# Kernel tuning notes

Measured on AMD Instinct MI355X. Metric: run time of the kernel, lower is better.

The kernel has to match this reference:

```python
import jax, jax.numpy as jnp
import numpy as np

N = 50000
E = 800000
D_IN = 96
D_OUT = 128


def setup_inputs() -> dict:
    key = jax.random.key(0)
    k1, k2, k3, k4, k5 = jax.random.split(key, 5)
    x = jax.random.normal(k1, (N, D_IN), dtype=jnp.float32)
    edge_index = jax.random.randint(k2, (2, E), 0, N, dtype=jnp.int32)
    s = 1.0 / np.sqrt(D_IN)
    # lin_l: applied to aggregated neighbor features (has bias in PyG SAGEConv)
    W_l = jax.random.uniform(k3, (D_OUT, D_IN), jnp.float32, -s, s)
    b_l = jax.random.uniform(k4, (D_OUT,), jnp.float32, -s, s)
    # lin_r: root/self weight (no bias)
    W_r = jax.random.uniform(k5, (D_OUT, D_IN), jnp.float32, -s, s)
    return {"x": x, "edge_index": edge_index, "W_l": W_l, "b_l": b_l, "W_r": W_r}


def reference(x, edge_index, W_l, b_l, W_r):
    src, dst = edge_index[0], edge_index[1]
    # gather source features, mean-aggregate onto targets
    msg = x[src]  # [E, D_IN]
    summed = jax.ops.segment_sum(msg, dst, num_segments=N)  # [N, D_IN]
    count = jax.ops.segment_sum(jnp.ones((E,), x.dtype), dst, num_segments=N)
    agg = summed / jnp.maximum(count, 1.0)[:, None]
    # SAGEConv: lin_l(agg) + lin_r(x), then layer-level ReLU
    out = agg @ W_l.T + b_l + x @ W_r.T
    return jax.nn.relu(out)
```

## Files before the change

kernel.cpp:

```cpp
#include <hip/hip_runtime.h>
#include <hip/hip_bf16.h>

#define N_NODES 50000
#define N_EDGES 800000
#define D_IN 96
#define D_OUT 128
#define CAP 64

#define NPB 64
#define N_BINS ((N_NODES + NPB - 1) / NPB)
#define CAP_SUB 24
#define PART_EPB 3125
#define PART_BLOCKS (N_EDGES / PART_EPB)
#define PART_SLOTS 13

#define CONV_THREADS (N_NODES * 12)
#define CONV_BLOCKS ((CONV_THREADS + 255) / 256)
#define WCONV_BLOCKS 12

#define AG_BLOCKS N_BINS
#define AH_PITCH 104

typedef unsigned short u16;
typedef __attribute__((ext_vector_type(8))) short short8;
typedef __attribute__((ext_vector_type(4))) float f32x4;

__device__ __forceinline__ u16 f2bf(float f) {
    unsigned u = __float_as_uint(f);
    unsigned r = (u + 0x7FFFu + ((u >> 16) & 1u)) >> 16;
    return (u16)r;
}
__device__ __forceinline__ float bf2f(u16 h) {
    return __uint_as_float(((unsigned)h) << 16);
}

__global__ __launch_bounds__(256) void sage_part_conv(
    const int* __restrict__ src,
    const int* __restrict__ dst,
    const float* __restrict__ x,
    const float* __restrict__ Wl,
    const float* __restrict__ Wr,
    u16* __restrict__ cnts,
    unsigned* __restrict__ binbuf,
    u16* __restrict__ xh,
    u16* __restrict__ Wfrag)
{
    __shared__ unsigned hist[N_BINS];
    __shared__ unsigned cur[N_BINS];

    const int b = blockIdx.x;
    const int tid = (int)threadIdx.x;

    if (b < PART_BLOCKS) {
        for (int i = tid; i < N_BINS; i += 256) { hist[i] = 0u; cur[i] = 0u; }
        __syncthreads();

        const int ebase = b * PART_EPB;
        const int e0 = ebase + tid;
        int d[PART_SLOTS], s[PART_SLOTS];
#pragma unroll
        for (int i = 0; i < PART_SLOTS; i++) {
            int valid = (tid + i * 256) < PART_EPB;
            int e = valid ? (e0 + i * 256) : ebase;
            d[i] = dst[e];
            s[i] = src[e];
        }
#pragma unroll
        for (int i = 0; i < PART_SLOTS; i++) {
            if ((tid + i * 256) < PART_EPB)
                atomicAdd(&hist[d[i] >> 6], 1u);
        }
        __syncthreads();
        for (int i = tid; i < N_BINS; i += 256)
            cnts[(size_t)i * PART_BLOCKS + b] = (u16)hist[i];
#pragma unroll
        for (int i = 0; i < PART_SLOTS; i++) {
            if ((tid + i * 256) < PART_EPB) {
                int bn = d[i] >> 6;
                unsigned dl = (unsigned)(d[i] & 63);
                unsigned loc = atomicAdd(&cur[bn], 1u);
                if (loc < CAP_SUB)
                    binbuf[((unsigned)bn * PART_BLOCKS + (unsigned)b) * CAP_SUB
                           + loc] = (dl << 16) | (unsigned)s[i];
            }
        }
    } else if (b < PART_BLOCKS + CONV_BLOCKS) {
        unsigned t = (unsigned)(b - PART_BLOCKS) * 256u + threadIdx.x;
        if (t >= (unsigned)CONV_THREADS) return;
        unsigned n = t / 12u;
        unsigned c8 = t - n * 12u;
        const float* p = x + (size_t)n * D_IN + c8 * 8u;
        short8 v;
#pragma unroll
        for (int i = 0; i < 8; i++) v[i] = (short)f2bf(p[i]);
        *(short8*)(xh + (size_t)n * D_IN + c8 * 8u) = v;
    } else {
        int idx = (b - PART_BLOCKS - CONV_BLOCKS) * 256 + tid;
        int j = idx / 24;
        int c8 = idx - j * 24;
        int kc = c8 >> 2;
        int quad = c8 & 3;
        const float* wsrc = (c8 < 12) ? (Wl + (size_t)j * D_IN + c8 * 8)
                                      : (Wr + (size_t)j * D_IN + (c8 - 12) * 8);
        int jt = j >> 4;
        int col = j & 15;
        short8 v;
#pragma unroll
        for (int i = 0; i < 8; i++) v[i] = (short)f2bf(wsrc[i]);
        *(short8*)(Wfrag + (((jt * 6 + kc) * 64) + col + 16 * quad) * 8) = v;
    }
}

__global__ __launch_bounds__(256) void sage_agg_gemm(
    const u16* __restrict__ xh,
    const u16* __restrict__ cnts,
    const unsigned* __restrict__ binbuf,
    const u16* __restrict__ Wfrag,
    const float* __restrict__ bl,
    float* __restrict__ out)
{
    __shared__ __align__(16) u16 bkt[NPB * CAP];
    __shared__ unsigned cnt_l[NPB];
    __shared__ u16 Ah[NPB * AH_PITCH];

    const int j = blockIdx.x;
    const int tid = (int)threadIdx.x;
    const int n0 = j * NPB;

    if (tid < NPB) cnt_l[tid] = 0u;
    __syncthreads();

    {
        unsigned cnt_t = cnts[(size_t)j * PART_BLOCKS + tid];
        const uint4* sc = (const uint4*)(binbuf
                          + ((size_t)j * PART_BLOCKS + tid) * CAP_SUB);
        uint4 q0 = sc[0], q1 = sc[1], q2 = sc[2], q3 = sc[3], q4 = sc[4], q5 = sc[5];
        unsigned buf[CAP_SUB];
        buf[0]=q0.x;  buf[1]=q0.y;  buf[2]=q0.z;  buf[3]=q0.w;
        buf[4]=q1.x;  buf[5]=q1.y;  buf[6]=q1.z;  buf[7]=q1.w;
        buf[8]=q2.x;  buf[9]=q2.y;  buf[10]=q2.z; buf[11]=q2.w;
        buf[12]=q3.x; buf[13]=q3.y; buf[14]=q3.z; buf[15]=q3.w;
        buf[16]=q4.x; buf[17]=q4.y; buf[18]=q4.z; buf[19]=q4.w;
        buf[20]=q5.x; buf[21]=q5.y; buf[22]=q5.z; buf[23]=q5.w;
        unsigned lim = cnt_t < CAP_SUB ? cnt_t : CAP_SUB;
#pragma unroll
        for (int e = 0; e < CAP_SUB; e++) {
            if ((unsigned)e < lim) {
                unsigned w = buf[e];
                unsigned r = w >> 16;
                unsigned p = atomicAdd(&cnt_l[r], 1u);
                if (p < CAP) bkt[r * CAP + p] = (u16)(w & 0xFFFFu);
            }
        }
    }
    __syncthreads();

#pragma unroll
    for (int rep = 0; rep < 3; rep++) {
        int task = rep * 256 + tid;
        int m = task / 12;
        int c8 = task - m * 12;
        int n = n0 + m;

        float acc[8];
#pragma unroll
        for (int i = 0; i < 8; i++) acc[i] = 0.0f;
        float invd = 0.0f;

        if (n < N_NODES) {
            int deg = (int)cnt_l[m];
            int degc = deg < CAP ? deg : CAP;
            const u16* brow = bkt + m * CAP;
            int e = 0;
            for (; e + 8 <= degc; e += 8) {
                short8 id = *(const short8*)(brow + e);
                short8 v[8];
#pragma unroll
                for (int q = 0; q < 8; q++) {
                    unsigned s = (u16)id[q];
                    v[q] = *(const short8*)(xh + s * (unsigned)D_IN + c8 * 8u);
                }
#pragma unroll
                for (int q = 0; q < 8; q++)
#pragma unroll
                    for (int i = 0; i < 8; i++) acc[i] += bf2f((u16)v[q][i]);
            }
            if (e + 4 <= degc) {
                unsigned s0 = brow[e + 0];
                unsigned s1 = brow[e + 1];
                unsigned s2 = brow[e + 2];
                unsigned s3 = brow[e + 3];
                short8 v0 = *(const short8*)(xh + s0 * (unsigned)D_IN + c8 * 8u);
                short8 v1 = *(const short8*)(xh + s1 * (unsigned)D_IN + c8 * 8u);
                short8 v2 = *(const short8*)(xh + s2 * (unsigned)D_IN + c8 * 8u);
                short8 v3 = *(const short8*)(xh + s3 * (unsigned)D_IN + c8 * 8u);
#pragma unroll
                for (int i = 0; i < 8; i++)
                    acc[i] += bf2f((u16)v0[i]) + bf2f((u16)v1[i])
                            + bf2f((u16)v2[i]) + bf2f((u16)v3[i]);
                e += 4;
            }
            for (; e < degc; e++) {
                unsigned s = brow[e];
                short8 v = *(const short8*)(xh + s * (unsigned)D_IN + c8 * 8u);
#pragma unroll
                for (int i = 0; i < 8; i++) acc[i] += bf2f((u16)v[i]);
            }
            invd = 1.0f / fmaxf((float)deg, 1.0f);
        }

        short8 o;
#pragma unroll
        for (int i = 0; i < 8; i++) o[i] = (short)f2bf(acc[i] * invd);
        *(short8*)(Ah + m * AH_PITCH + c8 * 8) = o;
    }
    __syncthreads();

    const int wave = tid >> 6;
    const int lane = tid & 63;
    const int m16 = lane & 15;
    const int quad = lane >> 4;
    const int tilebase = n0 + wave * 16;
    if (tilebase >= N_NODES) return;

    int nn = tilebase + m16;
    nn = nn < N_NODES ? nn : N_NODES - 1;

    const u16* arow = Ah + (wave * 16 + m16) * AH_PITCH + quad * 8;
    const u16* xrow = xh + (size_t)nn * D_IN + quad * 8;
    short8 a[6];
#pragma unroll
    for (int kc = 0; kc < 3; kc++) a[kc]     = *(const short8*)(arow + kc * 32);
#pragma unroll
    for (int kc = 0; kc < 3; kc++) a[3 + kc] = *(const short8*)(xrow + kc * 32);

#pragma unroll
    for (int jt = 0; jt < 8; jt++) {
        f32x4 acc = {0.0f, 0.0f, 0.0f, 0.0f};
#pragma unroll
        for (int kc = 0; kc < 6; kc++) {
            short8 bfrag = *(const short8*)(Wfrag + ((jt * 6 + kc) * 64 + lane) * 8);
            acc = __builtin_amdgcn_mfma_f32_16x16x32_bf16(a[kc], bfrag, acc, 0, 0, 0);
        }
        const int jj = jt * 16 + m16;
        const float bj = bl[jj];
#pragma unroll
        for (int r = 0; r < 4; r++) {
            int row = quad * 4 + r;
            int n = tilebase + row;
            if (n < N_NODES)
                out[(size_t)n * D_OUT + jj] = fmaxf(acc[r] + bj, 0.0f);
        }
    }
}

extern "C" void kernel_launch(void* const* d_in, const int* in_sizes, int n_in,
                              void* d_out, int out_size, void* d_ws, size_t ws_size,
                              hipStream_t stream) {
    const float* x   = (const float*)d_in[0];
    const int* eidx  = (const int*)d_in[1];
    const float* Wl  = (const float*)d_in[2];
    const float* bl  = (const float*)d_in[3];
    const float* Wr  = (const float*)d_in[4];
    float* out = (float*)d_out;

    const int* src = eidx;
    const int* dst = eidx + N_EDGES;

    char* ws = (char*)d_ws;
    unsigned* binbuf = (unsigned*)ws;
    u16*      cnts   = (u16*)(ws + 19218432);
    u16*      xh     = (u16*)(ws + 19618816);
    u16*      Wfrag  = (u16*)(ws + 29218816);

    {
        dim3 grid(PART_BLOCKS + CONV_BLOCKS + WCONV_BLOCKS);
        sage_part_conv<<<grid, 256, 0, stream>>>(src, dst, x, Wl, Wr,
                                                 cnts, binbuf, xh, Wfrag);
    }
    {
        dim3 grid(AG_BLOCKS);
        sage_agg_gemm<<<grid, 256, 0, stream>>>(xh, cnts, binbuf, Wfrag, bl, out);
    }
}
```

Baseline: 123.8 us.

## Double aggregation block threads, split edge lists across two halves with shared reduction

Launches the aggregation+GEMM kernel with 512 threads instead of 256. Each node-chunk's neighbor list is split into two halves handled by different threads, and the partial sums are combined through a new float shared-memory buffer. The MFMA phase now splits the output column tiles across twice as many waves, and the binbuf loads are skipped past each sub-bucket's count. This aims to raise memory-level parallelism in the gather. In exchange it adds extra shared memory (which may lower occupancy), extra __syncthreads inside the loop, and a partial-sum exchange.

```diff
diff --git a/kernel.cpp b/kernel.cpp
--- a/kernel.cpp
+++ b/kernel.cpp
@@ -20,6 +20,7 @@
 
 #define AG_BLOCKS N_BINS
 #define AH_PITCH 104
+#define S_PITCH 100
 
 typedef unsigned short u16;
 typedef __attribute__((ext_vector_type(8))) short short8;
@@ -111,7 +112,7 @@
     }
 }
 
-__global__ __launch_bounds__(256) void sage_agg_gemm(
+__global__ __launch_bounds__(512) void sage_agg_gemm(
     const u16* __restrict__ xh,
     const u16* __restrict__ cnts,
     const unsigned* __restrict__ binbuf,
@@ -121,7 +122,8 @@
 {
     __shared__ __align__(16) u16 bkt[NPB * CAP];
     __shared__ unsigned cnt_l[NPB];
-    __shared__ u16 Ah[NPB * AH_PITCH];
+    __shared__ __align__(16) float S[NPB * S_PITCH];
+    __shared__ __align__(16) u16 Ah[NPB * AH_PITCH];
 
     const int j = blockIdx.x;
     const int tid = (int)threadIdx.x;
@@ -130,11 +132,19 @@
     if (tid < NPB) cnt_l[tid] = 0u;
     __syncthreads();
 
-    {
+    if (tid < PART_BLOCKS) {
         unsigned cnt_t = cnts[(size_t)j * PART_BLOCKS + tid];
         const uint4* sc = (const uint4*)(binbuf
                           + ((size_t)j * PART_BLOCKS + tid) * CAP_SUB);
-        uint4 q0 = sc[0], q1 = sc[1], q2 = sc[2], q3 = sc[3], q4 = sc[4], q5 = sc[5];
+        unsigned lim = cnt_t < CAP_SUB ? cnt_t : CAP_SUB;
+        uint4 q0 = {0,0,0,0}, q1 = {0,0,0,0}, q2 = {0,0,0,0};
+        uint4 q3 = {0,0,0,0}, q4 = {0,0,0,0}, q5 = {0,0,0,0};
+        if (lim > 0)  q0 = sc[0];
+        if (lim > 4)  q1 = sc[1];
+        if (lim > 8)  q2 = sc[2];
+        if (lim > 12) q3 = sc[3];
+        if (lim > 16) q4 = sc[4];
+        if (lim > 20) q5 = sc[5];
         unsigned buf[CAP_SUB];
         buf[0]=q0.x;  buf[1]=q0.y;  buf[2]=q0.z;  buf[3]=q0.w;
         buf[4]=q1.x;  buf[5]=q1.y;  buf[6]=q1.z;  buf[7]=q1.w;
@@ -142,7 +152,6 @@
         buf[12]=q3.x; buf[13]=q3.y; buf[14]=q3.z; buf[15]=q3.w;
         buf[16]=q4.x; buf[17]=q4.y; buf[18]=q4.z; buf[19]=q4.w;
         buf[20]=q5.x; buf[21]=q5.y; buf[22]=q5.z; buf[23]=q5.w;
-        unsigned lim = cnt_t < CAP_SUB ? cnt_t : CAP_SUB;
 #pragma unroll
         for (int e = 0; e < CAP_SUB; e++) {
             if ((unsigned)e < lim) {
@@ -157,22 +166,27 @@
 
 #pragma unroll
     for (int rep = 0; rep < 3; rep++) {
-        int task = rep * 256 + tid;
-        int m = task / 12;
-        int c8 = task - m * 12;
+        int task = rep * 512 + tid;
+        int m = task / 24;
+        int rem = task - m * 24;
+        int half = rem >= 12 ? 1 : 0;
+        int c8 = rem - half * 12;
         int n = n0 + m;
 
         float acc[8];
 #pragma unroll
         for (int i = 0; i < 8; i++) acc[i] = 0.0f;
-        float invd = 0.0f;
+        int deg = 0;
 
         if (n < N_NODES) {
-            int deg = (int)cnt_l[m];
-            int degc = deg < CAP ? deg : CAP;
+            deg = (int)cnt_l[m];
+            int dc = deg < CAP ? deg : CAP;
+            int mid = ((dc >> 1) + 4) & ~7;
+            int e_lo = half ? mid : 0;
+            int e_hi = half ? dc : mid;
             const u16* brow = bkt + m * CAP;
-            int e = 0;
-            for (; e + 8 <= degc; e += 8) {
+            int e = e_lo;
+            for (; e + 8 <= e_hi; e += 8) {
                 short8 id = *(const short8*)(brow + e);
                 short8 v[8];
 #pragma unroll
@@ -185,7 +199,7 @@
 #pragma unroll
                     for (int i = 0; i < 8; i++) acc[i] += bf2f((u16)v[q][i]);
             }
-            if (e + 4 <= degc) {
+            if (e + 4 <= e_hi) {
                 unsigned s0 = brow[e + 0];
                 unsigned s1 = brow[e + 1];
                 unsigned s2 = brow[e + 2];
@@ -200,19 +214,29 @@
                             + bf2f((u16)v2[i]) + bf2f((u16)v3[i]);
                 e += 4;
             }
-            for (; e < degc; e++) {
+            for (; e < e_hi; e++) {
                 unsigned s = brow[e];
                 short8 v = *(const short8*)(xh + s * (unsigned)D_IN + c8 * 8u);
 #pragma unroll
                 for (int i = 0; i < 8; i++) acc[i] += bf2f((u16)v[i]);
             }
-            invd = 1.0f / fmaxf((float)deg, 1.0f);
-        }
-
-        short8 o;
-#pragma unroll
-        for (int i = 0; i < 8; i++) o[i] = (short)f2bf(acc[i] * invd);
-        *(short8*)(Ah + m * AH_PITCH + c8 * 8) = o;
+        }
+
+        if (half == 0) {
+            float* sp = S + m * S_PITCH + c8 * 8;
+            *(float4*)(sp)     = *(float4*)(&acc[0]);
+            *(float4*)(sp + 4) = *(float4*)(&acc[4]);
+        }
+        __syncthreads();
+        if (half == 1) {
+            const float* sp = S + m * S_PITCH + c8 * 8;
+            float invd = (n < N_NODES) ? 1.0f / fmaxf((float)deg, 1.0f) : 0.0f;
+            short8 o;
+#pragma unroll
+            for (int i = 0; i < 8; i++)
+                o[i] = (short)f2bf((acc[i] + sp[i]) * invd);
+            *(short8*)(Ah + m * AH_PITCH + c8 * 8) = o;
+        }
     }
     __syncthreads();
 
@@ -220,13 +244,15 @@
     const int lane = tid & 63;
     const int m16 = lane & 15;
     const int quad = lane >> 4;
-    const int tilebase = n0 + wave * 16;
+    const int tile = wave & 3;
+    const int jt0 = (wave >> 2) * 4;
+    const int tilebase = n0 + tile * 16;
     if (tilebase >= N_NODES) return;
 
     int nn = tilebase + m16;
     nn = nn < N_NODES ? nn : N_NODES - 1;
 
-    const u16* arow = Ah + (wave * 16 + m16) * AH_PITCH + quad * 8;
+    const u16* arow = Ah + (tile * 16 + m16) * AH_PITCH + quad * 8;
     const u16* xrow = xh + (size_t)nn * D_IN + quad * 8;
     short8 a[6];
 #pragma unroll
@@ -235,14 +261,15 @@
     for (int kc = 0; kc < 3; kc++) a[3 + kc] = *(const short8*)(xrow + kc * 32);
 
 #pragma unroll
-    for (int jt = 0; jt < 8; jt++) {
+    for (int jt = 0; jt < 4; jt++) {
+        const int jtt = jt0 + jt;
         f32x4 acc = {0.0f, 0.0f, 0.0f, 0.0f};
 #pragma unroll
         for (int kc = 0; kc < 6; kc++) {
-            short8 bfrag = *(const short8*)(Wfrag + ((jt * 6 + kc) * 64 + lane) * 8);
+            short8 bfrag = *(const short8*)(Wfrag + ((jtt * 6 + kc) * 64 + lane) * 8);
             acc = __builtin_amdgcn_mfma_f32_16x16x32_bf16(a[kc], bfrag, acc, 0, 0, 0);
         }
-        const int jj = jt * 16 + m16;
+        const int jj = jtt * 16 + m16;
         const float bj = bl[jj];
 #pragma unroll
         for (int r = 0; r < 4; r++) {
@@ -280,6 +307,6 @@
     }
     {
         dim3 grid(AG_BLOCKS);
-        sage_agg_gemm<<<grid, 256, 0, stream>>>(xh, cnts, binbuf, Wfrag, bl, out);
-    }
-}
+        sage_agg_gemm<<<grid, 512, 0, stream>>>(xh, cnts, binbuf, Wfrag, bl, out);
+    }
+}
```

Result: slower. 129.1 us (+4.3%).
